# Optimization experiments

Hardware: AMD Instinct MI355X
Metric: run time of the kernel (lower is better)

The kernel has to match this reference:

```python
import jax, jax.numpy as jnp
import numpy as np

B, N, D = 4, 2048, 1024
HEAD_DIMS = 128
NUM_HEADS = 8
PROJ = HEAD_DIMS * NUM_HEADS  # 1024


def setup_inputs() -> dict:
    key = jax.random.key(0)
    ks = jax.random.split(key, 5)
    # Weights stored as (in, out); xavier-normal-like scale
    def xavier(k, fan_in, fan_out):
        std = (2.0 / (fan_in + fan_out)) ** 0.5
        return jax.random.normal(k, (fan_in, fan_out), dtype=jnp.float32) * std
    return {
        "x": jax.random.normal(ks[0], (B, N, D), dtype=jnp.float32),
        "Wq": xavier(ks[1], D, PROJ),
        "Wk": xavier(ks[2], D, PROJ),
        "Wv": xavier(ks[3], D, PROJ),
        "Wo": xavier(ks[4], PROJ, PROJ),
    }


def reference(x, Wq, Wk, Wv, Wo):
    b, n, d = x.shape
    # QKV projections, split into heads: (b, h, n, hd)
    def split_heads(z):
        return z.reshape(b, n, NUM_HEADS, HEAD_DIMS).transpose(0, 2, 1, 3)
    q = split_heads(x @ Wq)
    k = split_heads(x @ Wk)
    v = split_heads(x @ Wv)
    scale = 1.0 / jnp.sqrt(jnp.float32(HEAD_DIMS))
    logits = jnp.einsum("bhqd,bhkd->bhqk", q, k) * scale
    weights = jax.nn.softmax(logits, axis=-1)
    out = jnp.einsum("bhqk,bhkd->bhqd", weights, v)
    out = out.transpose(0, 2, 1, 3).reshape(b, n, PROJ)
    return out @ Wo
```

## Files before the change

kernel.cpp:

```cpp
#include <hip/hip_runtime.h>
#include <hip/hip_bf16.h>


typedef __attribute__((ext_vector_type(8))) short short8;
typedef __attribute__((ext_vector_type(4))) short short4v;
typedef __attribute__((ext_vector_type(4))) float floatx4;
typedef __attribute__((ext_vector_type(8))) _Float16 half8;

#define MFMA_F16(a, b, c) __builtin_amdgcn_mfma_f32_16x16x32_f16( \
    __builtin_bit_cast(half8, (a)), __builtin_bit_cast(half8, (b)), (c), 0, 0, 0)

static constexpr int BATCH  = 4;
static constexpr int NHEADS = 8;
static constexpr int SEQ    = 2048;
static constexpr int HD     = 128;
static constexpr int DMODEL = 1024;
static constexpr int MROWS  = BATCH * SEQ;
static constexpr int NQKV   = 3 * DMODEL;

#define QSCALE2 0.12752283786512624f

static __device__ __forceinline__ short f16bits(float v) {
    return __builtin_bit_cast(short, (_Float16)v);
}

template <typename T>
static __device__ __forceinline__ short8 load8_f16(const T* p) {
    if constexpr (sizeof(T) == 2) {
        return *(const short8*)p;
    } else {
        const float4 f0 = *(const float4*)p;
        const float4 f1 = *(const float4*)(p + 4);
        short8 r;
        r[0] = f16bits(f0.x); r[1] = f16bits(f0.y);
        r[2] = f16bits(f0.z); r[3] = f16bits(f0.w);
        r[4] = f16bits(f1.x); r[5] = f16bits(f1.y);
        r[6] = f16bits(f1.z); r[7] = f16bits(f1.w);
        return r;
    }
}

static __device__ __forceinline__ void storeC(float* C, size_t idx, float v) {
    C[idx] = v;
}
static __device__ __forceinline__ void storeC(_Float16* C, size_t idx, float v) {
    C[idx] = (_Float16)v;
}

static __device__ __forceinline__ void gload16(const short* g, short* l) {
    __builtin_amdgcn_global_load_lds(
        (const __attribute__((address_space(1))) void*)g,
        (__attribute__((address_space(3))) void*)l, 16, 0, 0);
}

__global__ __launch_bounds__(256)
void prep(const float* __restrict__ x, short* __restrict__ xb,
          const float* __restrict__ W0, const float* __restrict__ W1,
          const float* __restrict__ W2, const float* __restrict__ W3,
          short* __restrict__ Wt, int K, int N)
{
    __shared__ short T[32][33];
    const int z = blockIdx.z;
    if (z >= 4) {
        const size_t chunk = ((size_t)(z - 4) * 1024 + blockIdx.y * 32 + blockIdx.x);
        const size_t i = (chunk * 256 + threadIdx.x) * 8;
        *(short8*)&xb[i] = load8_f16(&x[i]);
        return;
    }
    const float* W = (z == 0) ? W0 : (z == 1) ? W1 : (z == 2) ? W2 : W3;
    short* Wtz = Wt + (size_t)z * K * N;

    const int n0 = blockIdx.x * 32, k0 = blockIdx.y * 32;
    const int r = threadIdx.x >> 3, c4 = (threadIdx.x & 7) * 4;

    const float4 v = *(const float4*)&W[(size_t)(k0 + r) * N + n0 + c4];
    T[r][c4 + 0] = f16bits(v.x);
    T[r][c4 + 1] = f16bits(v.y);
    T[r][c4 + 2] = f16bits(v.z);
    T[r][c4 + 3] = f16bits(v.w);
    __syncthreads();

    short4v o;
    o[0] = T[c4 + 0][r]; o[1] = T[c4 + 1][r];
    o[2] = T[c4 + 2][r]; o[3] = T[c4 + 3][r];
    *(short4v*)&Wtz[(size_t)(n0 + r) * K + k0 + c4] = o;
}

__global__ __launch_bounds__(256)
void convx(const float* __restrict__ x, short* __restrict__ xb)
{
    const size_t i = ((size_t)blockIdx.x * 256 + threadIdx.x) * 8;
    *(short8*)&xb[i] = load8_f16(&x[i]);
}

__global__ __launch_bounds__(256)
void transpose_v(const short* __restrict__ V, short* __restrict__ Vt)
{
    __shared__ short T[64][72];
    const int s0 = blockIdx.x * 64;
    const int d0 = blockIdx.y * 64;
    const int bh = blockIdx.z;
    const short* Vi = V  + (size_t)bh * SEQ * HD;
    short*       Vo = Vt + (size_t)bh * HD * SEQ;

    const int r = threadIdx.x >> 3;
    const int c = threadIdx.x & 7;

    *(short8*)&T[r][c * 8]      = *(const short8*)&Vi[(size_t)(s0 + r) * HD + d0 + c * 8];
    *(short8*)&T[r + 32][c * 8] = *(const short8*)&Vi[(size_t)(s0 + r + 32) * HD + d0 + c * 8];
    __syncthreads();

    short8 o0, o1;
    #pragma unroll
    for (int j = 0; j < 8; ++j) {
        o0[j] = T[c * 8 + j][r];
        o1[j] = T[c * 8 + j][r + 32];
    }
    *(short8*)&Vo[(size_t)(d0 + r) * SEQ + s0 + c * 8]      = o0;
    *(short8*)&Vo[(size_t)(d0 + r + 32) * SEQ + s0 + c * 8] = o1;
}

template <typename OutT, bool QKV>
__global__ __launch_bounds__(256)
void gemm128(const short* __restrict__ A, const short* __restrict__ Bt,
             OutT* __restrict__ C, int M, int N, int K, size_t qkvStride)
{
    __shared__ __align__(16) short As[128 * 64];
    __shared__ __align__(16) short Bs[128 * 64];

    const int tid  = threadIdx.x;
    const int lane = tid & 63;
    const int w    = tid >> 6;
    const int quad = lane >> 4;
    const int l16  = lane & 15;

    const int m0 = blockIdx.x * 128;
    const int n0 = blockIdx.y * 128;
    const int wm = (w >> 1) * 64;
    const int wn = (w & 1) * 64;

    floatx4 acc[4][4] = {};

    const int srow   = tid >> 3;
    const int schunk = (tid & 7) ^ (srow & 7);
    const short* aG = A  + (size_t)(m0 + srow) * K + schunk * 8;
    const short* bG = Bt + (size_t)(n0 + srow) * K + schunk * 8;
    short* aL = As + tid * 8;
    short* bL = Bs + tid * 8;

    const int fsw = l16 & 7;

    for (int k0 = 0; k0 < K; k0 += 64) {
        __syncthreads();
        #pragma unroll
        for (int r = 0; r < 4; ++r) {
            gload16(aG + k0 + (size_t)(r * 32) * K, aL + r * 2048);
            gload16(bG + k0 + (size_t)(r * 32) * K, bL + r * 2048);
        }
        __syncthreads();

        #pragma unroll
        for (int kk = 0; kk < 2; ++kk) {
            short8 af[4], bf[4];
            #pragma unroll
            for (int mi = 0; mi < 4; ++mi)
                af[mi] = *(short8*)&As[(wm + mi * 16 + l16) * 64 +
                                       (((kk * 4 + quad) ^ fsw) * 8)];
            #pragma unroll
            for (int ni = 0; ni < 4; ++ni)
                bf[ni] = *(short8*)&Bs[(wn + ni * 16 + l16) * 64 +
                                       (((kk * 4 + quad) ^ fsw) * 8)];

            #pragma unroll
            for (int mi = 0; mi < 4; ++mi)
                #pragma unroll
                for (int ni = 0; ni < 4; ++ni)
                    acc[mi][ni] = MFMA_F16(af[mi], bf[ni], acc[mi][ni]);
        }
    }

    const size_t bigStride = qkvStride;
    #pragma unroll
    for (int mi = 0; mi < 4; ++mi)
        #pragma unroll
        for (int ni = 0; ni < 4; ++ni)
            #pragma unroll
            for (int r = 0; r < 4; ++r) {
                const int m = m0 + wm + mi * 16 + quad * 4 + r;
                const int n = n0 + wn + ni * 16 + l16;
                float v = acc[mi][ni][r];
                if constexpr (QKV) {
                    const int qkv = n >> 10, rem = n & 1023;
                    const int h = rem >> 7, d = rem & 127;
                    const int b = m >> 11, s = m & 2047;
                    if (qkv == 0) v *= QSCALE2;
                    storeC(C, (size_t)qkv * bigStride +
                              (((size_t)b * NHEADS + h) * SEQ + s) * HD + d, v);
                } else {
                    storeC(C, (size_t)m * N + n, v);
                }
            }
}

__global__ __launch_bounds__(512)
void attn_flash9(const short* __restrict__ Q, const short* __restrict__ K,
                 const short* __restrict__ Vt, _Float16* __restrict__ O)
{
    __shared__ __align__(16) short Ks[2][32 * 128];
    __shared__ __align__(16) short Vs[2][128 * 32];
    __shared__ __align__(16) short Plds[8][16 * 40];

    const int tid  = threadIdx.x;
    const int lane = tid & 63;
    const int w    = tid >> 6;
    const int quad = lane >> 4;
    const int l16  = lane & 15;

    const int h  = blockIdx.x & 7;
    const int qi = blockIdx.x >> 3;
    const int b  = blockIdx.y;
    const int q0 = qi * 128;

    const short* Qh  = Q  + (((size_t)b * NHEADS + h) * SEQ) * HD;
    const short* Kh  = K  + (((size_t)b * NHEADS + h) * SEQ) * HD;
    const short* Vth = Vt + (((size_t)b * NHEADS + h) * HD) * SEQ;

    const int qrow = q0 + w * 16 + l16;
    short8 qf[4];
    #pragma unroll
    for (int c = 0; c < 4; ++c)
        qf[c] = *(const short8*)&Qh[(size_t)qrow * HD + c * 32 + quad * 8];

    const int krow = tid >> 4, kp = tid & 15;
    const short* kG = Kh + (size_t)krow * HD + ((kp ^ (krow & 15)) * 8);
    const int vrow = tid >> 2, vp = tid & 3;
    const short* vG = Vth + (size_t)vrow * SEQ + ((vp ^ ((vrow >> 1) & 3)) * 8);
    short* kL0 = &Ks[0][0] + tid * 8;
    short* kL1 = &Ks[1][0] + tid * 8;
    short* vL0 = &Vs[0][0] + tid * 8;
    short* vL1 = &Vs[1][0] + tid * 8;

    float lrow[4] = {0.f, 0.f, 0.f, 0.f};
    floatx4 acc[8] = {};

    const int fswK = l16;
    const int fswV = (l16 >> 1) & 3;
    short* Pw = &Plds[w][0];

    gload16(kG, kL0);
    gload16(vG, vL0);
    kG += 32 * HD;
    vG += 32;

    for (int kt = 0; kt < SEQ; kt += 32) {
        const int cur = (kt >> 5) & 1;
        __syncthreads();
        if (kt + 32 < SEQ) {
            gload16(kG, cur ? kL0 : kL1);
            gload16(vG, cur ? vL0 : vL1);
            kG += 32 * HD;
            vG += 32;
        }
        const short* Kb = &Ks[cur][0];
        const short* Vb = &Vs[cur][0];

        floatx4 s0 = {}, s1 = {};
        #pragma unroll
        for (int c = 0; c < 4; ++c) {
            const int k_ = c * 4 + quad;
            short8 kf0 = *(short8*)&Kb[l16 * 128 + ((k_ ^ fswK) * 8)];
            short8 kf1 = *(short8*)&Kb[(16 + l16) * 128 + ((k_ ^ fswK) * 8)];
            s0 = MFMA_F16(qf[c], kf0, s0);
            s1 = MFMA_F16(qf[c], kf1, s1);
        }

        #pragma unroll
        for (int r = 0; r < 4; ++r) {
            const float p0 = exp2f(fminf(s0[r], 15.f));
            const float p1 = exp2f(fminf(s1[r], 15.f));
            lrow[r] += p0 + p1;
            Pw[(quad * 4 + r) * 40 + l16]      = f16bits(p0);
            Pw[(quad * 4 + r) * 40 + 16 + l16] = f16bits(p1);
        }
        short8 pf = *(short8*)&Pw[l16 * 40 + quad * 8];

        #pragma unroll
        for (int hc = 0; hc < 8; ++hc) {
            short8 vf = *(short8*)&Vb[(hc * 16 + l16) * 32 + ((quad ^ fswV) * 8)];
            acc[hc] = MFMA_F16(pf, vf, acc[hc]);
        }
    }

    #pragma unroll
    for (int r = 0; r < 4; ++r) {
        lrow[r] += __shfl_xor(lrow[r], 1);
        lrow[r] += __shfl_xor(lrow[r], 2);
        lrow[r] += __shfl_xor(lrow[r], 4);
        lrow[r] += __shfl_xor(lrow[r], 8);
    }

    #pragma unroll
    for (int hc = 0; hc < 8; ++hc)
        #pragma unroll
        for (int r = 0; r < 4; ++r) {
            const int row = q0 + w * 16 + quad * 4 + r;
            const float val = acc[hc][r] / fmaxf(lrow[r], 1e-30f);
            O[((size_t)b * SEQ + row) * DMODEL + h * HD + hc * 16 + l16] =
                (_Float16)val;
        }
}

template <typename AT, typename OutT>
__global__ __launch_bounds__(256)
void gemm64(const AT* __restrict__ A, const float* __restrict__ W,
            OutT* __restrict__ C, int M, int N, int K, int headsplit)
{
    __shared__ __align__(16) short As[64][32];
    __shared__ __align__(16) short Bs[64][32];

    const int tid  = threadIdx.x;
    const int lane = tid & 63;
    const int w    = tid >> 6;
    const int quad = lane >> 4;
    const int l16  = lane & 15;

    const int m0 = blockIdx.x * 64;
    const int n0 = blockIdx.y * 64;
    const int wm = (w >> 1) * 32;
    const int wn = (w & 1) * 32;

    floatx4 acc[2][2] = {};

    const int arow = tid >> 2, acol = (tid & 3) * 8;
    const int brow = tid >> 3, bcol = (tid & 7) * 8;

    const AT*    aptr = A + (size_t)(m0 + arow) * K + acol;
    const float* bptr = W + (size_t)brow * N + n0 + bcol;

    for (int k0 = 0; k0 < K; k0 += 32) {
        short8 av = load8_f16(aptr + k0);
        short8 bv = load8_f16(bptr + (size_t)k0 * N);
        __syncthreads();
        *(short8*)&As[arow][acol] = av;
        #pragma unroll
        for (int j = 0; j < 8; ++j)
            Bs[bcol + j][brow] = bv[j];
        __syncthreads();

        short8 af0 = *(short8*)&As[wm + l16][quad * 8];
        short8 af1 = *(short8*)&As[wm + 16 + l16][quad * 8];
        short8 bf0 = *(short8*)&Bs[wn + l16][quad * 8];
        short8 bf1 = *(short8*)&Bs[wn + 16 + l16][quad * 8];

        acc[0][0] = MFMA_F16(af0, bf0, acc[0][0]);
        acc[0][1] = MFMA_F16(af0, bf1, acc[0][1]);
        acc[1][0] = MFMA_F16(af1, bf0, acc[1][0]);
        acc[1][1] = MFMA_F16(af1, bf1, acc[1][1]);
    }

    #pragma unroll
    for (int mi = 0; mi < 2; ++mi)
        #pragma unroll
        for (int ni = 0; ni < 2; ++ni)
            #pragma unroll
            for (int r = 0; r < 4; ++r) {
                const int m = m0 + wm + mi * 16 + quad * 4 + r;
                const int n = n0 + wn + ni * 16 + l16;
                const float v = acc[mi][ni][r];
                if (headsplit) {
                    const int b = m >> 11, nn = m & 2047;
                    const int h = n >> 7,  d  = n & 127;
                    storeC(C, (((size_t)b * NHEADS + h) * SEQ + nn) * HD + d, v);
                } else {
                    storeC(C, (size_t)m * N + n, v);
                }
            }
}

__global__ __launch_bounds__(256)
void attn_flash(const short* __restrict__ Q, const short* __restrict__ K,
                const short* __restrict__ V, _Float16* __restrict__ O)
{
    __shared__ __align__(16) short Ksf[32][136];
    __shared__ __align__(16) short Vtl[HD][40];
    __shared__ __align__(16) short Pldsf[4][16][40];

    const int tid  = threadIdx.x;
    const int lane = tid & 63;
    const int w    = tid >> 6;
    const int quad = lane >> 4;
    const int l16  = lane & 15;

    const int q0 = blockIdx.x * 64;
    const int h  = blockIdx.y;
    const int b  = blockIdx.z;

    const size_t headoff = ((size_t)b * NHEADS + h) * SEQ * HD;
    const short* Qh = Q + headoff;
    const short* Kh = K + headoff;
    const short* Vh = V + headoff;

    const float scale = 0.08838834764831845f;

    const int qrow = q0 + w * 16 + l16;
    short8 qf[4];
    #pragma unroll
    for (int c = 0; c < 4; ++c)
        qf[c] = *(const short8*)&Qh[(size_t)qrow * HD + c * 32 + quad * 8];

    float mrow[4], lrow[4];
    #pragma unroll
    for (int r = 0; r < 4; ++r) { mrow[r] = -1e30f; lrow[r] = 0.f; }
    floatx4 acc[8] = {};

    const int krow = tid >> 4, kcol = (tid & 15) * 8;
    const int vkey = tid & 31;
    const int vhd  = (tid >> 5) * 16;

    for (int kt = 0; kt < SEQ; kt += 32) {
        const short* Kt = Kh + (size_t)kt * HD;
        short8 k0v = *(const short8*)(Kt + (size_t)tid * 8);
        short8 k1v = *(const short8*)(Kt + (size_t)(tid + 256) * 8);
        short8 v0 = *(const short8*)&Vh[(size_t)(kt + vkey) * HD + vhd];
        short8 v1 = *(const short8*)&Vh[(size_t)(kt + vkey) * HD + vhd + 8];

        __syncthreads();
        *(short8*)&Ksf[krow][kcol]      = k0v;
        *(short8*)&Ksf[krow + 16][kcol] = k1v;
        #pragma unroll
        for (int j = 0; j < 8; ++j) {
            Vtl[vhd + j][vkey]     = v0[j];
            Vtl[vhd + 8 + j][vkey] = v1[j];
        }
        __syncthreads();

        floatx4 s0 = {}, s1 = {};
        #pragma unroll
        for (int c = 0; c < 4; ++c) {
            short8 kf0 = *(short8*)&Ksf[l16][c * 32 + quad * 8];
            short8 kf1 = *(short8*)&Ksf[16 + l16][c * 32 + quad * 8];
            s0 = MFMA_F16(qf[c], kf0, s0);
            s1 = MFMA_F16(qf[c], kf1, s1);
        }

        float p0[4], p1[4], alpha[4];
        #pragma unroll
        for (int r = 0; r < 4; ++r) {
            const float a  = s0[r] * scale;
            const float bb = s1[r] * scale;
            float mx = fmaxf(a, bb);
            mx = fmaxf(mx, __shfl_xor(mx, 1));
            mx = fmaxf(mx, __shfl_xor(mx, 2));
            mx = fmaxf(mx, __shfl_xor(mx, 4));
            mx = fmaxf(mx, __shfl_xor(mx, 8));
            const float mnew = fmaxf(mrow[r], mx);
            alpha[r] = __expf(mrow[r] - mnew);
            mrow[r]  = mnew;
            p0[r] = __expf(a - mnew);
            p1[r] = __expf(bb - mnew);
            float rs = p0[r] + p1[r];
            rs += __shfl_xor(rs, 1);
            rs += __shfl_xor(rs, 2);
            rs += __shfl_xor(rs, 4);
            rs += __shfl_xor(rs, 8);
            lrow[r] = lrow[r] * alpha[r] + rs;
        }
        #pragma unroll
        for (int hc = 0; hc < 8; ++hc)
            #pragma unroll
            for (int r = 0; r < 4; ++r)
                acc[hc][r] *= alpha[r];

        #pragma unroll
        for (int r = 0; r < 4; ++r) {
            Pldsf[w][quad * 4 + r][l16]      = f16bits(p0[r]);
            Pldsf[w][quad * 4 + r][16 + l16] = f16bits(p1[r]);
        }
        __syncthreads();

        short8 pf = *(short8*)&Pldsf[w][l16][quad * 8];
        #pragma unroll
        for (int hc = 0; hc < 8; ++hc) {
            short8 vf = *(short8*)&Vtl[hc * 16 + l16][quad * 8];
            acc[hc] = MFMA_F16(pf, vf, acc[hc]);
        }
    }

    #pragma unroll
    for (int hc = 0; hc < 8; ++hc)
        #pragma unroll
        for (int r = 0; r < 4; ++r) {
            const int row = q0 + w * 16 + quad * 4 + r;
            const float val = acc[hc][r] / fmaxf(lrow[r], 1e-30f);
            O[((size_t)b * SEQ + row) * DMODEL + h * HD + hc * 16 + l16] =
                (_Float16)val;
        }
}

extern "C" void kernel_launch(void* const* d_in, const int* in_sizes, int n_in,
                              void* d_out, int out_size, void* d_ws, size_t ws_size,
                              hipStream_t stream)
{
    const float* x  = (const float*)d_in[0];
    const float* Wq = (const float*)d_in[1];
    const float* Wk = (const float*)d_in[2];
    const float* Wv = (const float*)d_in[3];
    const float* Wo = (const float*)d_in[4];
    float* out = (float*)d_out;

    const size_t bufElems = (size_t)MROWS * DMODEL;
    const size_t batElems = (size_t)SEQ * DMODEL;
    const size_t MiB = 1024 * 1024;
    dim3 tt(256);

    if (ws_size >= 72 * MiB) {
        short* xb    = (short*)d_ws;
        short* Qb    = xb + bufElems;
        short* Kb    = xb + 2 * bufElems;
        short* Vn    = xb + 3 * bufElems;
        short* Wtall = xb + 4 * bufElems;
        short* Wto   = Wtall + 3 * (size_t)DMODEL * DMODEL;
        short* VtG   = xb;
        short* Ab    = Vn;

        prep<<<dim3(32, 32, 8), tt, 0, stream>>>(
            x, xb, Wq, Wk, Wv, Wo, Wtall, DMODEL, DMODEL);

        gemm128<_Float16, true><<<dim3(MROWS / 128, NQKV / 128), tt, 0, stream>>>(
            xb, Wtall, (_Float16*)Qb, MROWS, NQKV, DMODEL, bufElems);

        transpose_v<<<dim3(SEQ / 64, HD / 64, BATCH * NHEADS), tt, 0, stream>>>(Vn, VtG);

        attn_flash9<<<dim3(NHEADS * (SEQ / 128), BATCH), dim3(512), 0, stream>>>(
            Qb, Kb, VtG, (_Float16*)Ab);

        gemm128<float, false><<<dim3(MROWS / 128, DMODEL / 128), tt, 0, stream>>>(
            Ab, Wto, out, MROWS, DMODEL, DMODEL, 0);
    } else if (ws_size >= 64 * MiB) {
        short* xb    = (short*)d_ws;
        short* Qb    = xb + 2 * batElems;
        short* Kb    = Qb + 4 * batElems;
        short* Vn    = Kb + 4 * batElems;
        short* Wtall = Vn + 4 * batElems;
        short* Wto   = Wtall + 3 * (size_t)DMODEL * DMODEL;

        prep<<<dim3(32, 32, 4), tt, 0, stream>>>(
            nullptr, nullptr, Wq, Wk, Wv, Wo, Wtall, DMODEL, DMODEL);

        for (int half = 0; half < 2; ++half) {
            const size_t off = (size_t)half * 2 * batElems;
            convx<<<dim3(2048), tt, 0, stream>>>(x + off, xb);
            gemm128<_Float16, true><<<dim3(32, NQKV / 128), tt, 0, stream>>>(
                xb, Wtall, (_Float16*)(Qb + off), 2 * SEQ, NQKV, DMODEL,
                4 * batElems);
        }
        for (int half = 0; half < 2; ++half) {
            const size_t off = (size_t)half * 2 * batElems;
            transpose_v<<<dim3(SEQ / 64, HD / 64, 2 * NHEADS), tt, 0, stream>>>(
                Vn + off, xb);
            attn_flash9<<<dim3(NHEADS * (SEQ / 128), 2), dim3(512), 0, stream>>>(
                Qb + off, Kb + off, xb, (_Float16*)(Vn + off));
        }
        gemm128<float, false><<<dim3(MROWS / 128, DMODEL / 128), tt, 0, stream>>>(
            Vn, Wto, out, MROWS, DMODEL, DMODEL, 0);
    } else if (ws_size >= 24 * MiB) {
        short* xb    = (short*)d_ws;
        short* Qb    = xb + batElems;
        short* Kb    = xb + 2 * batElems;
        short* Vb    = xb + 3 * batElems;
        short* Wtall = xb + 4 * batElems;
        short* Wto   = Wtall + 3 * (size_t)DMODEL * DMODEL;

        prep<<<dim3(32, 32, 4), tt, 0, stream>>>(
            nullptr, nullptr, Wq, Wk, Wv, Wo, Wtall, DMODEL, DMODEL);

        for (int b = 0; b < BATCH; ++b) {
            convx<<<dim3(1024), tt, 0, stream>>>(x + (size_t)b * batElems, xb);
            gemm128<_Float16, true><<<dim3(SEQ / 128, NQKV / 128), tt, 0, stream>>>(
                xb, Wtall, (_Float16*)Qb, SEQ, NQKV, DMODEL, batElems);
            transpose_v<<<dim3(SEQ / 64, HD / 64, NHEADS), tt, 0, stream>>>(Vb, xb);
            attn_flash9<<<dim3(NHEADS * (SEQ / 128), 1), dim3(512), 0, stream>>>(
                Qb, Kb, xb, (_Float16*)Vb);
            gemm128<float, false><<<dim3(SEQ / 128, DMODEL / 128), tt, 0, stream>>>(
                Vb, Wto, out + (size_t)b * batElems, SEQ, DMODEL, DMODEL, 0);
        }
    } else {
        short* Qb = (short*)d_ws;
        short* Kb = Qb + batElems;
        short* Vb = Qb + 2 * batElems;
        short* Ab = Qb + 3 * batElems;

        dim3 gg(SEQ / 64, DMODEL / 64);
        for (int b = 0; b < BATCH; ++b) {
            const float* xb_ = x + (size_t)b * batElems;
            gemm64<float, _Float16><<<gg, tt, 0, stream>>>(
                xb_, Wq, (_Float16*)Qb, SEQ, DMODEL, DMODEL, 1);
            gemm64<float, _Float16><<<gg, tt, 0, stream>>>(
                xb_, Wk, (_Float16*)Kb, SEQ, DMODEL, DMODEL, 1);
            gemm64<float, _Float16><<<gg, tt, 0, stream>>>(
                xb_, Wv, (_Float16*)Vb, SEQ, DMODEL, DMODEL, 1);
            attn_flash<<<dim3(SEQ / 64, NHEADS, 1), tt, 0, stream>>>(
                Qb, Kb, Vb, (_Float16*)Ab);
            gemm64<short, float><<<gg, tt, 0, stream>>>(
                Ab, Wo, out + (size_t)b * batElems, SEQ, DMODEL, DMODEL, 0);
        }
    }
}
```

Baseline: 289.5 us.

## Shrink attention blocks to 256 threads and compute row sums via MFMA

The flash attention kernel now uses 256-thread blocks covering 64 query rows instead of 512 threads covering 128, so twice as many blocks are launched. Each thread stages two K and two V chunks per tile, and the loop is unrolled over two explicit LDS buffers. The softmax denominator is now accumulated with an extra MFMA against a vector of ones, which removes the scalar adds and the end-of-kernel cross-lane shuffles. exp2f with clamping is replaced by the raw hardware exp2 builtin. The trade-off is more K/V reloads per query row, one extra MFMA per tile, and no longer clamping the logits against overflow.

```diff
diff --git a/kernel.cpp b/kernel.cpp
--- a/kernel.cpp
+++ b/kernel.cpp
@@ -179,7 +179,6 @@
         }
     }
 
-    const size_t bigStride = qkvStride;
     #pragma unroll
     for (int mi = 0; mi < 4; ++mi)
         #pragma unroll
@@ -194,7 +193,7 @@
                     const int h = rem >> 7, d = rem & 127;
                     const int b = m >> 11, s = m & 2047;
                     if (qkv == 0) v *= QSCALE2;
-                    storeC(C, (size_t)qkv * bigStride +
+                    storeC(C, (size_t)qkv * qkvStride +
                               (((size_t)b * NHEADS + h) * SEQ + s) * HD + d, v);
                 } else {
                     storeC(C, (size_t)m * N + n, v);
@@ -202,13 +201,13 @@
             }
 }
 
-__global__ __launch_bounds__(512)
-void attn_flash9(const short* __restrict__ Q, const short* __restrict__ K,
-                 const short* __restrict__ Vt, _Float16* __restrict__ O)
+__global__ __launch_bounds__(256)
+void attn_flash10(const short* __restrict__ Q, const short* __restrict__ K,
+                  const short* __restrict__ Vt, _Float16* __restrict__ O)
 {
     __shared__ __align__(16) short Ks[2][32 * 128];
     __shared__ __align__(16) short Vs[2][128 * 32];
-    __shared__ __align__(16) short Plds[8][16 * 40];
+    __shared__ __align__(16) short Plds[4][16 * 40];
 
     const int tid  = threadIdx.x;
     const int lane = tid & 63;
@@ -219,7 +218,7 @@
     const int h  = blockIdx.x & 7;
     const int qi = blockIdx.x >> 3;
     const int b  = blockIdx.y;
-    const int q0 = qi * 128;
+    const int q0 = qi * 64;
 
     const short* Qh  = Q  + (((size_t)b * NHEADS + h) * SEQ) * HD;
     const short* Kh  = K  + (((size_t)b * NHEADS + h) * SEQ) * HD;
@@ -231,82 +230,84 @@
     for (int c = 0; c < 4; ++c)
         qf[c] = *(const short8*)&Qh[(size_t)qrow * HD + c * 32 + quad * 8];
 
-    const int krow = tid >> 4, kp = tid & 15;
-    const short* kG = Kh + (size_t)krow * HD + ((kp ^ (krow & 15)) * 8);
-    const int vrow = tid >> 2, vp = tid & 3;
-    const short* vG = Vth + (size_t)vrow * SEQ + ((vp ^ ((vrow >> 1) & 3)) * 8);
-    short* kL0 = &Ks[0][0] + tid * 8;
-    short* kL1 = &Ks[1][0] + tid * 8;
-    short* vL0 = &Vs[0][0] + tid * 8;
-    short* vL1 = &Vs[1][0] + tid * 8;
-
-    float lrow[4] = {0.f, 0.f, 0.f, 0.f};
+    const int kr0 = tid >> 4, kc0 = tid & 15;
+    const int kr1 = kr0 + 16;
+    const short* kGa = Kh + (size_t)kr0 * HD + ((kc0 ^ (kr0 & 15)) * 8);
+    const short* kGb = Kh + (size_t)kr1 * HD + ((kc0 ^ (kr1 & 15)) * 8);
+    const int vr0 = tid >> 2, vp0 = tid & 3;
+    const short* vGa = Vth + (size_t)vr0 * SEQ + ((vp0 ^ ((vr0 >> 1) & 3)) * 8);
+    const short* vGb = Vth + (size_t)(vr0 + 64) * SEQ + ((vp0 ^ ((vr0 >> 1) & 3)) * 8);
+
     floatx4 acc[8] = {};
-
-    const int fswK = l16;
+    floatx4 acc9 = {};
+
+    short8 ones;
+    #pragma unroll
+    for (int j = 0; j < 8; ++j) ones[j] = 0x3C00;
+
     const int fswV = (l16 >> 1) & 3;
     short* Pw = &Plds[w][0];
 
-    gload16(kG, kL0);
-    gload16(vG, vL0);
-    kG += 32 * HD;
-    vG += 32;
-
-    for (int kt = 0; kt < SEQ; kt += 32) {
-        const int cur = (kt >> 5) & 1;
-        __syncthreads();
-        if (kt + 32 < SEQ) {
-            gload16(kG, cur ? kL0 : kL1);
-            gload16(vG, cur ? vL0 : vL1);
-            kG += 32 * HD;
-            vG += 32;
-        }
-        const short* Kb = &Ks[cur][0];
-        const short* Vb = &Vs[cur][0];
-
+    auto STAGE = [&](short* kDst, short* vDst, int tile) {
+        const size_t ko = (size_t)tile * 32 * HD;
+        const size_t vo = (size_t)tile * 32;
+        gload16(kGa + ko, kDst + tid * 8);
+        gload16(kGb + ko, kDst + (tid + 256) * 8);
+        gload16(vGa + vo, vDst + tid * 8);
+        gload16(vGb + vo, vDst + (tid + 256) * 8);
+    };
+
+    auto COMPUTE = [&](const short* Kb, const short* Vb) {
         floatx4 s0 = {}, s1 = {};
         #pragma unroll
         for (int c = 0; c < 4; ++c) {
             const int k_ = c * 4 + quad;
-            short8 kf0 = *(short8*)&Kb[l16 * 128 + ((k_ ^ fswK) * 8)];
-            short8 kf1 = *(short8*)&Kb[(16 + l16) * 128 + ((k_ ^ fswK) * 8)];
+            short8 kf0 = *(short8*)&Kb[l16 * 128 + ((k_ ^ l16) * 8)];
+            short8 kf1 = *(short8*)&Kb[(16 + l16) * 128 + ((k_ ^ l16) * 8)];
             s0 = MFMA_F16(qf[c], kf0, s0);
             s1 = MFMA_F16(qf[c], kf1, s1);
         }
-
         #pragma unroll
         for (int r = 0; r < 4; ++r) {
-            const float p0 = exp2f(fminf(s0[r], 15.f));
-            const float p1 = exp2f(fminf(s1[r], 15.f));
-            lrow[r] += p0 + p1;
+            const float p0 = __builtin_amdgcn_exp2f(s0[r]);
+            const float p1 = __builtin_amdgcn_exp2f(s1[r]);
             Pw[(quad * 4 + r) * 40 + l16]      = f16bits(p0);
             Pw[(quad * 4 + r) * 40 + 16 + l16] = f16bits(p1);
         }
         short8 pf = *(short8*)&Pw[l16 * 40 + quad * 8];
-
+        acc9 = MFMA_F16(pf, ones, acc9);
         #pragma unroll
         for (int hc = 0; hc < 8; ++hc) {
             short8 vf = *(short8*)&Vb[(hc * 16 + l16) * 32 + ((quad ^ fswV) * 8)];
             acc[hc] = MFMA_F16(pf, vf, acc[hc]);
         }
-    }
-
-    #pragma unroll
-    for (int r = 0; r < 4; ++r) {
-        lrow[r] += __shfl_xor(lrow[r], 1);
-        lrow[r] += __shfl_xor(lrow[r], 2);
-        lrow[r] += __shfl_xor(lrow[r], 4);
-        lrow[r] += __shfl_xor(lrow[r], 8);
-    }
+    };
+
+    STAGE(&Ks[0][0], &Vs[0][0], 0);
+
+    for (int kt = 0; kt < SEQ; kt += 64) {
+        const int t = kt >> 5;
+        __syncthreads();
+        STAGE(&Ks[1][0], &Vs[1][0], t + 1);
+        COMPUTE(&Ks[0][0], &Vs[0][0]);
+        __syncthreads();
+        if (kt + 64 < SEQ)
+            STAGE(&Ks[0][0], &Vs[0][0], t + 2);
+        COMPUTE(&Ks[1][0], &Vs[1][0]);
+    }
+
+    float rinv[4];
+    #pragma unroll
+    for (int r = 0; r < 4; ++r)
+        rinv[r] = 1.0f / fmaxf(acc9[r], 1e-30f);
 
     #pragma unroll
     for (int hc = 0; hc < 8; ++hc)
         #pragma unroll
         for (int r = 0; r < 4; ++r) {
             const int row = q0 + w * 16 + quad * 4 + r;
-            const float val = acc[hc][r] / fmaxf(lrow[r], 1e-30f);
             O[((size_t)b * SEQ + row) * DMODEL + h * HD + hc * 16 + l16] =
-                (_Float16)val;
+                (_Float16)(acc[hc][r] * rinv[r]);
         }
 }
 
@@ -531,7 +532,7 @@
 
         transpose_v<<<dim3(SEQ / 64, HD / 64, BATCH * NHEADS), tt, 0, stream>>>(Vn, VtG);
 
-        attn_flash9<<<dim3(NHEADS * (SEQ / 128), BATCH), dim3(512), 0, stream>>>(
+        attn_flash10<<<dim3(NHEADS * (SEQ / 64), BATCH), tt, 0, stream>>>(
             Qb, Kb, VtG, (_Float16*)Ab);
 
         gemm128<float, false><<<dim3(MROWS / 128, DMODEL / 128), tt, 0, stream>>>(
@@ -558,7 +559,7 @@
             const size_t off = (size_t)half * 2 * batElems;
             transpose_v<<<dim3(SEQ / 64, HD / 64, 2 * NHEADS), tt, 0, stream>>>(
                 Vn + off, xb);
-            attn_flash9<<<dim3(NHEADS * (SEQ / 128), 2), dim3(512), 0, stream>>>(
+            attn_flash10<<<dim3(NHEADS * (SEQ / 64), 2), tt, 0, stream>>>(
                 Qb + off, Kb + off, xb, (_Float16*)(Vn + off));
         }
         gemm128<float, false><<<dim3(MROWS / 128, DMODEL / 128), tt, 0, stream>>>(
@@ -579,7 +580,7 @@
             gemm128<_Float16, true><<<dim3(SEQ / 128, NQKV / 128), tt, 0, stream>>>(
                 xb, Wtall, (_Float16*)Qb, SEQ, NQKV, DMODEL, batElems);
             transpose_v<<<dim3(SEQ / 64, HD / 64, NHEADS), tt, 0, stream>>>(Vb, xb);
-            attn_flash9<<<dim3(NHEADS * (SEQ / 128), 1), dim3(512), 0, stream>>>(
+            attn_flash10<<<dim3(NHEADS * (SEQ / 64), 1), tt, 0, stream>>>(
                 Qb, Kb, xb, (_Float16*)Vb);
             gemm128<float, false><<<dim3(SEQ / 128, DMODEL / 128), tt, 0, stream>>>(
                 Vb, Wto, out + (size_t)b * batElems, SEQ, DMODEL, DMODEL, 0);
```

After: 290.9 us. About the same (+0.5%).
